# Performance work log

Hardware: AMD Instinct MI355X
Metric: run time of the kernel (lower is better)

The kernel has to match this reference:

```python
import jax, jax.numpy as jnp
import numpy as np

EPS = 1e-8        # LinearGELU eps
LN_EPS = 1e-5     # LayerNorm eps
NUM_HEADS = 16
DIM = 1024
HIDDEN = 4096
B, N = 4, 785


def _lin(x, xj, w, lw, b=None, lb=None):
    # LinearLinear: primal linear + JVP wrt input and tangent params (lw, lb)
    y = x @ w.T
    yj = xj @ w.T + x @ lw.T
    if b is not None:
        y = y + b
    if lb is not None:
        yj = yj + lb
    return y, yj


def _ln(x, xj, w, b, lw, lb):
    # LinearLayerNorm forward + manual JVP (matches torch source exactly)
    mean = x.mean(-1, keepdims=True)
    xc = x - mean
    var = (xc * xc).mean(-1, keepdims=True)
    std = jnp.sqrt(var + LN_EPS)
    xhat = xc / std
    out = xhat * w + b
    t1 = xhat * lw + lb                              # tangent wrt affine params
    mj = xj.mean(-1, keepdims=True)
    xjc = xj - mj
    a = xjc * std
    corr = 2.0 * (xc * xjc).mean(-1, keepdims=True)
    bterm = (0.5 / std) * corr * xc
    c = (1.0 / std) ** 2 * (a - bterm)
    return out, t1 + c * w


def _gelu(x, xj):
    # exact (erf) GELU; jvp uses gelu(x)/(x+EPS) + x*pdf(x) as in source
    out = 0.5 * x * (1.0 + jax.lax.erf(x * np.float32(1.0 / np.sqrt(2.0))))
    pdf = jnp.exp(-0.5 * x * x) * np.float32(1.0 / np.sqrt(2.0 * np.pi))
    return out, xj * (out / (x + EPS) + x * pdf)


def _attn(x, xj, qkv_w, qkv_lw, proj_w, proj_b, proj_lw, proj_lb):
    Bb, Nn, C = x.shape
    H = NUM_HEADS
    D = C // H
    scale = np.float32(D) ** -0.5
    qkv, qkv_j = _lin(x, xj, qkv_w, qkv_lw)  # [B,N,3C], qkv_bias=False
    def split(t):
        return t.reshape(Bb, Nn, 3, H, D).transpose(2, 0, 3, 1, 4)
    q, k, v = split(qkv)
    qj, kj, vj = split(qkv_j)
    q = q * scale
    qj = qj * scale
    attn = jax.nn.softmax(jnp.einsum('bhnd,bhmd->bhnm', q, k), axis=-1)
    out = jnp.einsum('bhnm,bhmd->bhnd', attn, v)
    # softmax JVP: dm = A_jvp + B_jvp; filter = dm*attn - rowsum(dm*attn)*attn
    dm = jnp.einsum('bhnd,bhmd->bhnm', qj, k) + jnp.einsum('bhnd,bhmd->bhnm', q, kj)
    f = dm * attn
    filt = f - f.sum(-1, keepdims=True) * attn  # == diag(dm @ attn^T) * attn correction
    out_j = jnp.einsum('bhnm,bhmd->bhnd', filt, v) + jnp.einsum('bhnm,bhmd->bhnd', attn, vj)
    out = out.transpose(0, 2, 1, 3).reshape(Bb, Nn, C)
    out_j = out_j.transpose(0, 2, 1, 3).reshape(Bb, Nn, C)
    return _lin(out, out_j, proj_w, proj_lw, proj_b, proj_lb)


def setup_inputs() -> dict:
    keys = jax.random.split(jax.random.key(0), 32)
    ki = iter(keys)
    def nrm(shape, s=0.02):
        return (jax.random.normal(next(ki), shape, jnp.float32) * s).astype(jnp.float32)
    d, h = DIM, HIDDEN
    inp = {
        'input': jax.random.normal(next(ki), (B, N, d), jnp.float32),
        'input_jvp': jax.random.normal(next(ki), (B, N, d), jnp.float32),
        'n1_w': 1.0 + nrm((d,), 0.1), 'n1_b': nrm((d,), 0.1),
        'n1_lw': nrm((d,), 0.1), 'n1_lb': nrm((d,), 0.1),
        'qkv_w': nrm((3 * d, d)), 'qkv_lw': nrm((3 * d, d)),
        'proj_w': nrm((d, d)), 'proj_b': nrm((d,), 0.1),
        'proj_lw': nrm((d, d)), 'proj_lb': nrm((d,), 0.1),
        'n2_w': 1.0 + nrm((d,), 0.1), 'n2_b': nrm((d,), 0.1),
        'n2_lw': nrm((d,), 0.1), 'n2_lb': nrm((d,), 0.1),
        'fc1_w': nrm((h, d)), 'fc1_b': nrm((h,), 0.1),
        'fc1_lw': nrm((h, d)), 'fc1_lb': nrm((h,), 0.1),
        'fc2_w': nrm((d, h)), 'fc2_b': nrm((d,), 0.1),
        'fc2_lw': nrm((d, h)), 'fc2_lb': nrm((d,), 0.1),
    }
    return inp


def reference(input, input_jvp, n1_w, n1_b, n1_lw, n1_lb, qkv_w, qkv_lw,
              proj_w, proj_b, proj_lw, proj_lb, n2_w, n2_b, n2_lw, n2_lb,
              fc1_w, fc1_b, fc1_lw, fc1_lb, fc2_w, fc2_b, fc2_lw, fc2_lb):
    x, xj = _ln(input, input_jvp, n1_w, n1_b, n1_lw, n1_lb)
    x, xj = _attn(x, xj, qkv_w, qkv_lw, proj_w, proj_b, proj_lw, proj_lb)
    x = x + input
    xj = xj + input_jvp
    i2, i2j = x, xj
    x, xj = _ln(x, xj, n2_w, n2_b, n2_lw, n2_lb)
    x, xj = _lin(x, xj, fc1_w, fc1_lw, fc1_b, fc1_lb)
    x, xj = _gelu(x, xj)
    x, xj = _lin(x, xj, fc2_w, fc2_lw, fc2_b, fc2_lb)
    return (x + i2, xj + i2j)
```

## Files before the change

kernel.cpp:

```cpp
#include <hip/hip_runtime.h>
#include <hip/hip_bf16.h>

typedef unsigned short u16;
typedef unsigned int   u32;

#define MP     3328
#define MREAL  3140
#define DIMC   1024
#define H3C    3072
#define HIDC   4096
#define NKV    785
#define SLEN   896

typedef __bf16 bf16x8 __attribute__((ext_vector_type(8)));
typedef float  f32x4  __attribute__((ext_vector_type(4)));

#define MFMA(d,a,b) (d) = __builtin_amdgcn_mfma_f32_16x16x32_bf16((a),(b),(d),0,0,0)

__device__ __forceinline__ u16 f2bf(float f){
  u32 u = __builtin_bit_cast(u32, f);
  return (u16)((u + 0x7fffu + ((u >> 16) & 1u)) >> 16);
}
__device__ __forceinline__ float bf2f(u16 h){
  return __builtin_bit_cast(float, (u32)h << 16);
}
__device__ __forceinline__ void gload16(const u16* g, u16* l){
  __builtin_amdgcn_global_load_lds(
      (const __attribute__((address_space(1))) void*)g,
      (__attribute__((address_space(3))) void*)l, 16, 0, 0);
}
__device__ __forceinline__ float wsum(float v){
  #pragma unroll
  for (int o = 32; o >= 1; o >>= 1) v += __shfl_xor(v, o);
  return v;
}

__global__ __launch_bounds__(256) void cvt_k(const float* __restrict__ in,
                                             u16* __restrict__ out, int n){
  int i = (blockIdx.x * 256 + threadIdx.x) * 4;
  if (i >= n) return;
  float4 v = *(const float4*)(in + i);
  ushort4 o4;
  o4.x = f2bf(v.x); o4.y = f2bf(v.y); o4.z = f2bf(v.z); o4.w = f2bf(v.w);
  *(ushort4*)(out + i) = o4;
}

__global__ __launch_bounds__(256) void ln_jvp_k(
    const float* __restrict__ x, const float* __restrict__ xj,
    const float* __restrict__ w, const float* __restrict__ b,
    const float* __restrict__ lw, const float* __restrict__ lb,
    u16* __restrict__ out, u16* __restrict__ outj)
{
  const int row = blockIdx.x, t = threadIdx.x;
  const size_t ro = (size_t)row * DIMC;
  if (row >= MREAL){
    for (int i = t; i < DIMC; i += 256){ out[ro+i] = 0; outj[ro+i] = 0; }
    return;
  }
  const float4 v  = ((const float4*)(x  + ro))[t];
  const float4 vj = ((const float4*)(xj + ro))[t];
  float sx  = v.x+v.y+v.z+v.w;
  float sxx = v.x*v.x+v.y*v.y+v.z*v.z+v.w*v.w;
  float sj  = vj.x+vj.y+vj.z+vj.w;
  float sxj = v.x*vj.x+v.y*vj.y+v.z*vj.z+v.w*vj.w;
  __shared__ __attribute__((aligned(64))) float red[4][4];
  sx = wsum(sx); sxx = wsum(sxx); sj = wsum(sj); sxj = wsum(sxj);
  const int wid = t>>6, lane = t&63;
  if (lane == 0){ red[wid][0]=sx; red[wid][1]=sxx; red[wid][2]=sj; red[wid][3]=sxj; }
  __syncthreads();
  sx  = red[0][0]+red[1][0]+red[2][0]+red[3][0];
  sxx = red[0][1]+red[1][1]+red[2][1]+red[3][1];
  sj  = red[0][2]+red[1][2]+red[2][2]+red[3][2];
  sxj = red[0][3]+red[1][3]+red[2][3]+red[3][3];
  const float inv  = 1.0f/1024.0f;
  const float mean = sx*inv, meanj = sj*inv;
  const float var  = sxx*inv - mean*mean;
  const float cov  = sxj*inv - mean*meanj;
  const float rstd = rsqrtf(var + 1e-5f);
  const float r3   = rstd*rstd*rstd;
  const float4 wv  = ((const float4*)w)[t];
  const float4 bv  = ((const float4*)b)[t];
  const float4 lwv = ((const float4*)lw)[t];
  const float4 lbv = ((const float4*)lb)[t];
  const float xs[4]  = {v.x,v.y,v.z,v.w},   xjs[4] = {vj.x,vj.y,vj.z,vj.w};
  const float wss[4] = {wv.x,wv.y,wv.z,wv.w}, bs[4] = {bv.x,bv.y,bv.z,bv.w};
  const float lws[4] = {lwv.x,lwv.y,lwv.z,lwv.w}, lbs[4] = {lbv.x,lbv.y,lbv.z,lbv.w};
  const int i0 = t*4;
  #pragma unroll
  for (int e = 0; e < 4; e++){
    const float xc = xs[e]-mean, xjc = xjs[e]-meanj;
    const float xhat = xc*rstd;
    const float cc = xjc*rstd - xc*cov*r3;
    out [ro+i0+e] = f2bf(xhat*wss[e] + bs[e]);
    outj[ro+i0+e] = f2bf(xhat*lws[e] + lbs[e] + cc*wss[e]);
  }
}

template<int EPI>
__global__ __launch_bounds__(512, 2) void gemm_jvp_wide_k(
    const u16* __restrict__ A, const u16* __restrict__ Aj, int lda,
    const u16* __restrict__ B, const u16* __restrict__ Bj, int K,
    const float* __restrict__ bias, const float* __restrict__ biasj,
    void* __restrict__ Yv, void* __restrict__ Yjv, int ldy)
{
  __shared__ __attribute__((aligned(128))) u16 lds[3][24576];
  const int tid = threadIdx.x, wid = tid>>6, lane = tid&63;
  const int l4 = lane>>4, l15 = lane&15;
  const int m0 = blockIdx.y*256, n0 = blockIdx.x*128;
  f32x4 accY[4][4], accJ[4][4];
  #pragma unroll
  for (int i = 0; i < 4; i++)
    #pragma unroll
    for (int j = 0; j < 4; j++){
      accY[i][j] = (f32x4){0.f,0.f,0.f,0.f};
      accJ[i][j] = (f32x4){0.f,0.f,0.f,0.f};
    }
  const int boA0 = tid*16,        boA1 = (512+tid)*16;
  const int sbA0 = boA0 ^ (((boA0>>7)&7)<<4);
  const int sbA1 = boA1 ^ (((boA1>>7)&7)<<4);
  const int rA0 = sbA0>>6, cA0 = (sbA0&63)>>1;
  const int rA1 = sbA1>>6, cA1 = (sbA1&63)>>1;
  const int boB = tid*16;
  const int sbB = boB ^ (((boB>>7)&7)<<4);
  const int rB = sbB>>6, cB = (sbB&63)>>1;
  const u16* srcA0  = A  + (size_t)(m0+rA0)*lda + cA0;
  const u16* srcA1  = A  + (size_t)(m0+rA1)*lda + cA1;
  const u16* srcAj0 = Aj + (size_t)(m0+rA0)*lda + cA0;
  const u16* srcAj1 = Aj + (size_t)(m0+rA1)*lda + cA1;
  const u16* srcB   = B  + (size_t)(n0+rB)*K + cB;
  const u16* srcBj  = Bj + (size_t)(n0+rB)*K + cB;
  const int dA0 = tid*8, dA1 = (512+tid)*8, dB = tid*8;
  const int wr = wid>>1, wc = wid&1;
  int aoff[4], boff[4];
  #pragma unroll
  for (int i = 0; i < 4; i++){
    int ab_ = (wr*64 + i*16 + l15)*64 + l4*16;
    aoff[i] = ab_ ^ (((ab_>>7)&7)<<4);
    int bb_ = (wc*64 + i*16 + l15)*64 + l4*16;
    boff[i] = bb_ ^ (((bb_>>7)&7)<<4);
  }
  auto STAGE = [&](int buf, int t){
    const int k0 = t<<5;
    u16* Lb = &lds[buf][0];
    gload16(srcA0 +k0, Lb + dA0);
    gload16(srcA1 +k0, Lb + dA1);
    gload16(srcAj0+k0, Lb + 8192 + dA0);
    gload16(srcAj1+k0, Lb + 8192 + dA1);
    gload16(srcB  +k0, Lb + 16384 + dB);
    gload16(srcBj +k0, Lb + 20480 + dB);
  };
  const int nt = K >> 5;
  STAGE(0, 0);
  STAGE(1, 1);
  for (int t = 0; t < nt; t++){
    if (t + 1 < nt) asm volatile("s_waitcnt vmcnt(6)" ::: "memory");
    else            asm volatile("s_waitcnt vmcnt(0)" ::: "memory");
    __builtin_amdgcn_s_barrier();
    if (t + 2 < nt) STAGE((t+2)%3, t+2);
    const char* Lb = (const char*)&lds[t%3][0];
    bf16x8 af[4], ajf[4], bbf[4], bjf[4];
    #pragma unroll
    for (int i = 0; i < 4; i++){
      af[i]  = *(const bf16x8*)(Lb + aoff[i]);
      ajf[i] = *(const bf16x8*)(Lb + 16384 + aoff[i]);
      bbf[i] = *(const bf16x8*)(Lb + 32768 + boff[i]);
      bjf[i] = *(const bf16x8*)(Lb + 40960 + boff[i]);
    }
    __builtin_amdgcn_s_setprio(1);
    #pragma unroll
    for (int i = 0; i < 4; i++)
      #pragma unroll
      for (int j = 0; j < 4; j++){
        MFMA(accY[i][j], af[i],  bbf[j]);
        MFMA(accJ[i][j], ajf[i], bbf[j]);
        MFMA(accJ[i][j], af[i],  bjf[j]);
      }
    __builtin_amdgcn_s_setprio(0);
  }
  const int mb = m0 + wr*64 + (l4<<2);
  const int nb = n0 + wc*64 + l15;
  #pragma unroll
  for (int i = 0; i < 4; i++)
    #pragma unroll
    for (int j = 0; j < 4; j++)
      #pragma unroll
      for (int r = 0; r < 4; r++){
        const int m = mb + i*16 + r, n = nb + j*16;
        float y = accY[i][j][r], yj = accJ[i][j][r];
        if (EPI == 0){
          ((u16*)Yv )[(size_t)m*ldy+n] = f2bf(y);
          ((u16*)Yjv)[(size_t)m*ldy+n] = f2bf(yj);
        } else {
          y  += bias[n];
          yj += biasj[n];
          const float ge  = 0.5f*y*(1.0f + erff(y*0.70710678118654752f));
          const float pdf = __expf(-0.5f*y*y)*0.3989422804014327f;
          const float gj  = yj*(ge/(y + 1e-8f) + y*pdf);
          ((u16*)Yv )[(size_t)m*ldy+n] = f2bf(ge);
          ((u16*)Yjv)[(size_t)m*ldy+n] = f2bf(gj);
        }
      }
}

template<int EPI>
__global__ __launch_bounds__(256) void gemm_jvp_k(
    const u16* __restrict__ A, const u16* __restrict__ Aj, int lda,
    const u16* __restrict__ B, const u16* __restrict__ Bj, int K,
    const float* __restrict__ bias, const float* __restrict__ biasj,
    const float* __restrict__ res, const float* __restrict__ resj,
    void* __restrict__ Yv, void* __restrict__ Yjv, int ldy, int mwrite)
{
  __shared__ __attribute__((aligned(128))) u16 lds[2][4][128*32];
  const int tid = threadIdx.x, wid = tid>>6, lane = tid&63;
  const int m0 = blockIdx.y*128, n0 = blockIdx.x*128;
  f32x4 accY[4][4], accJ[4][4];
  #pragma unroll
  for (int i = 0; i < 4; i++)
    #pragma unroll
    for (int j = 0; j < 4; j++){
      accY[i][j] = (f32x4){0.f,0.f,0.f,0.f};
      accJ[i][j] = (f32x4){0.f,0.f,0.f,0.f};
    }
  const int bo0 = wid*1024 + lane*16;
  const int bo1 = bo0 + 4096;
  const int sb0 = bo0 ^ (((bo0>>7)&7)<<4);
  const int sb1 = bo1 ^ (((bo1>>7)&7)<<4);
  const int r0 = sb0>>6, c0 = (sb0&63)>>1;
  const int r1 = sb1>>6, c1 = (sb1&63)>>1;
  const u16* A0  = A  + (size_t)(m0+r0)*lda + c0;
  const u16* A1  = A  + (size_t)(m0+r1)*lda + c1;
  const u16* Aj0 = Aj + (size_t)(m0+r0)*lda + c0;
  const u16* Aj1 = Aj + (size_t)(m0+r1)*lda + c1;
  const u16* B0  = B  + (size_t)(n0+r0)*K + c0;
  const u16* B1  = B  + (size_t)(n0+r1)*K + c1;
  const u16* Bj0 = Bj + (size_t)(n0+r0)*K + c0;
  const u16* Bj1 = Bj + (size_t)(n0+r1)*K + c1;
  const int kq = (lane>>4)<<3;
  const int ar = (wid>>1)*64 + (lane&15);
  const int bc = (wid&1)*64 + (lane&15);
  int aoff[4], boff[4];
  #pragma unroll
  for (int i = 0; i < 4; i++){
    int ab_ = (ar+i*16)*64 + (kq<<1);
    aoff[i] = ab_ ^ (((ab_>>7)&7)<<4);
    int bb_ = (bc+i*16)*64 + (kq<<1);
    boff[i] = bb_ ^ (((bb_>>7)&7)<<4);
  }
  auto STAGE = [&](int buf, int k0){
    u16* p0 = &lds[buf][0][0];
    gload16(A0 +k0, p0+(bo0>>1)); gload16(A1 +k0, p0+(bo1>>1));
    u16* p1 = &lds[buf][1][0];
    gload16(Aj0+k0, p1+(bo0>>1)); gload16(Aj1+k0, p1+(bo1>>1));
    u16* p2 = &lds[buf][2][0];
    gload16(B0 +k0, p2+(bo0>>1)); gload16(B1 +k0, p2+(bo1>>1));
    u16* p3 = &lds[buf][3][0];
    gload16(Bj0+k0, p3+(bo0>>1)); gload16(Bj1+k0, p3+(bo1>>1));
  };
  const int nt = K >> 5;
  STAGE(0, 0);
  __syncthreads();
  int cur = 0;
  for (int t = 0; t < nt; t++){
    if (t + 1 < nt) STAGE(cur^1, (t+1)<<5);
    const char* lAb  = (const char*)&lds[cur][0][0];
    const char* lAjb = (const char*)&lds[cur][1][0];
    const char* lBb  = (const char*)&lds[cur][2][0];
    const char* lBjb = (const char*)&lds[cur][3][0];
    bf16x8 af[4], ajf[4], bbf[4], bjf[4];
    #pragma unroll
    for (int i = 0; i < 4; i++){
      af[i]  = *(const bf16x8*)(lAb  + aoff[i]);
      ajf[i] = *(const bf16x8*)(lAjb + aoff[i]);
      bbf[i] = *(const bf16x8*)(lBb  + boff[i]);
      bjf[i] = *(const bf16x8*)(lBjb + boff[i]);
    }
    __builtin_amdgcn_s_setprio(1);
    #pragma unroll
    for (int i = 0; i < 4; i++)
      #pragma unroll
      for (int j = 0; j < 4; j++){
        MFMA(accY[i][j], af[i],  bbf[j]);
        MFMA(accJ[i][j], ajf[i], bbf[j]);
        MFMA(accJ[i][j], af[i],  bjf[j]);
      }
    __builtin_amdgcn_s_setprio(0);
    __syncthreads();
    cur ^= 1;
  }
  const int mb = m0 + (wid>>1)*64 + ((lane>>4)<<2);
  const int nb = n0 + (wid&1)*64 + (lane&15);
  #pragma unroll
  for (int i = 0; i < 4; i++)
    #pragma unroll
    for (int j = 0; j < 4; j++)
      #pragma unroll
      for (int r = 0; r < 4; r++){
        const int m = mb + i*16 + r, n = nb + j*16;
        float y = accY[i][j][r], yj = accJ[i][j][r];
        if (EPI == 0){
          ((u16*)Yv )[(size_t)m*ldy+n] = f2bf(y);
          ((u16*)Yjv)[(size_t)m*ldy+n] = f2bf(yj);
        } else if (EPI == 1){
          if (m < mwrite){
            y  += bias[n]  + res [(size_t)m*ldy+n];
            yj += biasj[n] + resj[(size_t)m*ldy+n];
            ((float*)Yv )[(size_t)m*ldy+n] = y;
            ((float*)Yjv)[(size_t)m*ldy+n] = yj;
          }
        } else {
          y  += bias[n];
          yj += biasj[n];
          const float ge  = 0.5f*y*(1.0f + erff(y*0.70710678118654752f));
          const float pdf = __expf(-0.5f*y*y)*0.3989422804014327f;
          const float gj  = yj*(ge/(y + 1e-8f) + y*pdf);
          ((u16*)Yv )[(size_t)m*ldy+n] = f2bf(ge);
          ((u16*)Yjv)[(size_t)m*ldy+n] = f2bf(gj);
        }
      }
}

__global__ __launch_bounds__(256) void transpose_v_k(
    const u16* __restrict__ qkvb, const u16* __restrict__ qkvjb,
    u16* __restrict__ vT, u16* __restrict__ vjT)
{
  __shared__ __attribute__((aligned(64))) u16 tl[64][80];
  __shared__ __attribute__((aligned(64))) u16 tlj[64][80];
  const int kt = blockIdx.x, bh = blockIdx.y;
  const int b = bh>>4, h = bh&15;
  const int t = threadIdx.x;
  const int kv = t>>2, dd = (t&3)*16;
  const int kvg = kt*64 + kv;
  if (kvg < NKV){
    const u16* s0 = qkvb  + (size_t)(b*NKV+kvg)*H3C + 2048 + h*64 + dd;
    const u16* s1 = qkvjb + (size_t)(b*NKV+kvg)*H3C + 2048 + h*64 + dd;
    *(uint4*)&tl [kv][dd]   = *(const uint4*)s0;
    *(uint4*)&tl [kv][dd+8] = *(const uint4*)(s0+8);
    *(uint4*)&tlj[kv][dd]   = *(const uint4*)s1;
    *(uint4*)&tlj[kv][dd+8] = *(const uint4*)(s1+8);
  } else {
    uint4 z = {0,0,0,0};
    *(uint4*)&tl [kv][dd] = z; *(uint4*)&tl [kv][dd+8] = z;
    *(uint4*)&tlj[kv][dd] = z; *(uint4*)&tlj[kv][dd+8] = z;
  }
  __syncthreads();
  const int d = t>>2, kc = (t&3)*16;
  u16* d0 = vT  + ((size_t)bh*64 + d)*SLEN + kt*64 + kc;
  u16* d1 = vjT + ((size_t)bh*64 + d)*SLEN + kt*64 + kc;
  #pragma unroll
  for (int e = 0; e < 16; e++){ d0[e] = tl[kc+e][d]; d1[e] = tlj[kc+e][d]; }
}

__global__ __launch_bounds__(256) void flash_attn_jvp_k(
    const u16* __restrict__ qkvb, const u16* __restrict__ qkvjb,
    const u16* __restrict__ vT, const u16* __restrict__ vjT,
    u16* __restrict__ o, u16* __restrict__ oj)
{
  __shared__ __attribute__((aligned(64))) u16 lK  [64*64];
  __shared__ __attribute__((aligned(64))) u16 lKj [64*64];
  __shared__ __attribute__((aligned(64))) u16 lvT [64*64];
  __shared__ __attribute__((aligned(64))) u16 lvjT[64*64];
  __shared__ __attribute__((aligned(64))) u16 pl  [128*64];
  __shared__ __attribute__((aligned(64))) u16 pdl [128*64];
  const int tid = threadIdx.x, wid = tid>>6, lane = tid&63;
  const int l4 = lane>>4, l15 = lane&15;
  const int qt = blockIdx.x, bh = blockIdx.y, b = bh>>4, h = bh&15;

  bf16x8 qf[2][2], qjf[2][2];
  {
    const size_t qrb = (size_t)b*NKV + qt*128 + wid*32;
    #pragma unroll
    for (int i = 0; i < 2; i++){
      const size_t ro = (qrb + i*16 + l15)*H3C + h*64;
      #pragma unroll
      for (int ks = 0; ks < 2; ks++){
        qf [i][ks] = *(const bf16x8*)(qkvb  + ro + ks*32 + l4*8);
        qjf[i][ks] = *(const bf16x8*)(qkvjb + ro + ks*32 + l4*8);
      }
    }
  }
  float m_st[2][4], l_st[2][4], g_st[2][4];
  f32x4 PO[2][4], PTJ[2][4];
  #pragma unroll
  for (int i = 0; i < 2; i++)
    #pragma unroll
    for (int r = 0; r < 4; r++){
      m_st[i][r] = -1e30f; l_st[i][r] = 0.f; g_st[i][r] = 0.f;
    }
  #pragma unroll
  for (int i = 0; i < 2; i++)
    #pragma unroll
    for (int j = 0; j < 4; j++){
      PO[i][j] = (f32x4){0.f,0.f,0.f,0.f};
      PTJ[i][j] = (f32x4){0.f,0.f,0.f,0.f};
    }
  const char* lKb   = (const char*)lK;
  const char* lKjb  = (const char*)lKj;
  const char* lvTb  = (const char*)lvT;
  const char* lvjTb = (const char*)lvjT;
  char* plb  = (char*)pl;
  char* pdlb = (char*)pdl;

  for (int t = 0; t < 13; t++){
    #pragma unroll
    for (int rnd = 0; rnd < 2; rnd++){
      const int gidx = rnd*256 + tid;
      const int row = gidx>>3, c = gidx&7;
      const int cs = c ^ (row&7);
      const size_t ksrc = (size_t)(b*NKV + t*64 + row)*H3C + 1024 + h*64 + cs*8;
      gload16(qkvb  + ksrc, lK  + gidx*8);
      gload16(qkvjb + ksrc, lKj + gidx*8);
      const size_t vsrc = ((size_t)bh*64 + row)*SLEN + t*64 + cs*8;
      gload16(vT  + vsrc, lvT  + gidx*8);
      gload16(vjT + vsrc, lvjT + gidx*8);
    }
    __syncthreads();

    #pragma unroll
    for (int i = 0; i < 2; i++){
      f32x4 s[4], dm[4];
      #pragma unroll
      for (int j = 0; j < 4; j++){
        s[j] = (f32x4){0.f,0.f,0.f,0.f};
        dm[j] = (f32x4){0.f,0.f,0.f,0.f};
      }
      #pragma unroll
      for (int ks = 0; ks < 2; ks++){
        #pragma unroll
        for (int j = 0; j < 4; j++){
          const int row = j*16 + l15;
          const int byt = (row*128 + ks*64 + l4*16) ^ ((row&7)<<4);
          const bf16x8 kf  = *(const bf16x8*)(lKb  + byt);
          const bf16x8 kjf = *(const bf16x8*)(lKjb + byt);
          MFMA(s[j],  qf[i][ks],  kf);
          MFMA(dm[j], qjf[i][ks], kf);
          MFMA(dm[j], qf[i][ks],  kjf);
        }
      }
      float tm[4] = {-1e30f,-1e30f,-1e30f,-1e30f};
      #pragma unroll
      for (int j = 0; j < 4; j++){
        const int colg = t*64 + j*16 + l15;
        #pragma unroll
        for (int r = 0; r < 4; r++){
          float sv = s[j][r]*0.125f;
          if (colg >= NKV) sv = -1e30f;
          s[j][r] = sv;
          dm[j][r] *= 0.125f;
          tm[r] = fmaxf(tm[r], sv);
        }
      }
      #pragma unroll
      for (int r = 0; r < 4; r++){
        float v = tm[r];
        v = fmaxf(v, __shfl_xor(v, 1));
        v = fmaxf(v, __shfl_xor(v, 2));
        v = fmaxf(v, __shfl_xor(v, 4));
        v = fmaxf(v, __shfl_xor(v, 8));
        const float mn = fmaxf(m_st[i][r], v);
        const float sc = __expf(m_st[i][r] - mn);
        m_st[i][r] = mn;
        l_st[i][r] *= sc;
        g_st[i][r] *= sc;
        #pragma unroll
        for (int j = 0; j < 4; j++){ PO[i][j][r] *= sc; PTJ[i][j][r] *= sc; }
      }
      float ps[4] = {0.f,0.f,0.f,0.f}, pds[4] = {0.f,0.f,0.f,0.f};
      #pragma unroll
      for (int j = 0; j < 4; j++){
        const int col = j*16 + l15;
        #pragma unroll
        for (int r = 0; r < 4; r++){
          const float p  = __expf(s[j][r] - m_st[i][r]);
          const float pd = p * dm[j][r];
          ps[r] += p; pds[r] += pd;
          const int row = wid*32 + i*16 + l4*4 + r;
          const int byt = (row*128 + col*2) ^ ((row&7)<<4);
          *(u16*)(plb  + byt) = f2bf(p);
          *(u16*)(pdlb + byt) = f2bf(pd);
        }
      }
      #pragma unroll
      for (int r = 0; r < 4; r++){
        float v = ps[r], w = pds[r];
        v += __shfl_xor(v, 1); w += __shfl_xor(w, 1);
        v += __shfl_xor(v, 2); w += __shfl_xor(w, 2);
        v += __shfl_xor(v, 4); w += __shfl_xor(w, 4);
        v += __shfl_xor(v, 8); w += __shfl_xor(w, 8);
        l_st[i][r] += v; g_st[i][r] += w;
      }
    }

    #pragma unroll
    for (int ks = 0; ks < 2; ks++){
      bf16x8 pa[2], pda[2];
      #pragma unroll
      for (int i = 0; i < 2; i++){
        const int row = wid*32 + i*16 + l15;
        const int byt = (row*128 + ks*64 + l4*16) ^ ((row&7)<<4);
        pa[i]  = *(const bf16x8*)(plb  + byt);
        pda[i] = *(const bf16x8*)(pdlb + byt);
      }
      #pragma unroll
      for (int j = 0; j < 4; j++){
        const int row = j*16 + l15;
        const int byt = (row*128 + ks*64 + l4*16) ^ ((row&7)<<4);
        const bf16x8 vb  = *(const bf16x8*)(lvTb  + byt);
        const bf16x8 vjb = *(const bf16x8*)(lvjTb + byt);
        #pragma unroll
        for (int i = 0; i < 2; i++){
          MFMA(PO[i][j],  pa[i],  vb);
          MFMA(PTJ[i][j], pda[i], vb);
          MFMA(PTJ[i][j], pa[i],  vjb);
        }
      }
    }
    __syncthreads();
  }

  #pragma unroll
  for (int i = 0; i < 2; i++)
    #pragma unroll
    for (int r = 0; r < 4; r++){
      const int ql = qt*128 + wid*32 + i*16 + l4*4 + r;
      if (ql < NKV){
        const float rl = 1.0f / l_st[i][r];
        const float gg = g_st[i][r] * rl;
        #pragma unroll
        for (int j = 0; j < 4; j++){
          const size_t oo = ((size_t)b*NKV + ql)*DIMC + h*64 + j*16 + l15;
          const float po = PO[i][j][r] * rl;
          o [oo] = f2bf(po);
          oj[oo] = f2bf(PTJ[i][j][r]*rl - gg*po);
        }
      }
    }
}

extern "C" void kernel_launch(void* const* d_in, const int* in_sizes, int n_in,
                              void* d_out, int out_size, void* d_ws, size_t ws_size,
                              hipStream_t stream)
{
  (void)in_sizes; (void)n_in; (void)out_size;
  const float* input   = (const float*)d_in[0];
  const float* inputj  = (const float*)d_in[1];
  const float* n1_w    = (const float*)d_in[2];
  const float* n1_b    = (const float*)d_in[3];
  const float* n1_lw   = (const float*)d_in[4];
  const float* n1_lb   = (const float*)d_in[5];
  const float* qkv_w   = (const float*)d_in[6];
  const float* qkv_lw  = (const float*)d_in[7];
  const float* proj_w  = (const float*)d_in[8];
  const float* proj_b  = (const float*)d_in[9];
  const float* proj_lw = (const float*)d_in[10];
  const float* proj_lb = (const float*)d_in[11];
  const float* n2_w    = (const float*)d_in[12];
  const float* n2_b    = (const float*)d_in[13];
  const float* n2_lw   = (const float*)d_in[14];
  const float* n2_lb   = (const float*)d_in[15];
  const float* fc1_w   = (const float*)d_in[16];
  const float* fc1_b   = (const float*)d_in[17];
  const float* fc1_lw  = (const float*)d_in[18];
  const float* fc1_lb  = (const float*)d_in[19];
  const float* fc2_w   = (const float*)d_in[20];
  const float* fc2_b   = (const float*)d_in[21];
  const float* fc2_lw  = (const float*)d_in[22];
  const float* fc2_lb  = (const float*)d_in[23];

  const size_t SZ_W      = 2u*4194304u*2u;
  const size_t SZ_ARENA1 = 2u*(size_t)MP*HIDC*2u;
  const size_t SZ_VT     = (size_t)64*64*SLEN*2u;
  const size_t SZ_ARENA2 = 2u*SZ_VT;
  const size_t SZ_ARENA3 = 2u*(size_t)MP*DIMC*2u;
  const size_t SZ_X2     = (size_t)MP*DIMC*4u;
  const size_t NEEDED = SZ_W + SZ_ARENA1 + SZ_ARENA2 + SZ_ARENA3 + 2u*SZ_X2 + 4096u;
  if (ws_size < NEEDED) return;

  char* base = (char*)d_ws;
  size_t off = 0;
  auto ab = [&](size_t bytes)->char*{
    char* p = base + off;
    off += bytes; off = (off + 255) & ~(size_t)255;
    return p;
  };
  char* Wslot  = ab(SZ_W);
  char* arena1 = ab(SZ_ARENA1);
  char* arena2 = ab(SZ_ARENA2);
  char* arena3 = ab(SZ_ARENA3);
  float* x2  = (float*)ab(SZ_X2);
  float* x2j = (float*)ab(SZ_X2);

  u16* wbuf  = (u16*)Wslot;
  u16* wjbuf = wbuf + 4194304;
  u16* qkvb  = (u16*)arena1;
  u16* qkvjb = qkvb + (size_t)MP*H3C;
  u16* hb    = (u16*)arena1;
  u16* hjb   = hb + (size_t)MP*HIDC;
  u16* vT    = (u16*)arena2;
  u16* vjT   = vT + (size_t)64*64*SLEN;
  u16* x3b   = (u16*)arena2;
  u16* x3jb  = x3b + (size_t)MP*DIMC;
  u16* x1b   = (u16*)arena3;
  u16* x1jb  = x1b + (size_t)MP*DIMC;
  u16* ob    = (u16*)arena3;
  u16* ojb   = ob + (size_t)MP*DIMC;

  auto cvt = [&](const float* src, u16* dst, int n){
    cvt_k<<<dim3((n + 1023)/1024), 256, 0, stream>>>(src, dst, n);
  };

  ln_jvp_k<<<dim3(MP), 256, 0, stream>>>(input, inputj, n1_w, n1_b, n1_lw, n1_lb,
                                         x1b, x1jb);
  cvt(qkv_w, wbuf, H3C*DIMC); cvt(qkv_lw, wjbuf, H3C*DIMC);
  gemm_jvp_wide_k<0><<<dim3(H3C/128, MP/256), 512, 0, stream>>>(
      x1b, x1jb, DIMC, wbuf, wjbuf, DIMC, nullptr, nullptr,
      qkvb, qkvjb, H3C);
  transpose_v_k<<<dim3(14, 64), 256, 0, stream>>>(qkvb, qkvjb, vT, vjT);
  flash_attn_jvp_k<<<dim3(7, 64), 256, 0, stream>>>(qkvb, qkvjb, vT, vjT, ob, ojb);
  cvt(proj_w, wbuf, DIMC*DIMC); cvt(proj_lw, wjbuf, DIMC*DIMC);
  gemm_jvp_k<1><<<dim3(DIMC/128, MP/128), 256, 0, stream>>>(
      ob, ojb, DIMC, wbuf, wjbuf, DIMC, proj_b, proj_lb, input, inputj,
      x2, x2j, DIMC, MREAL);
  ln_jvp_k<<<dim3(MP), 256, 0, stream>>>(x2, x2j, n2_w, n2_b, n2_lw, n2_lb,
                                         x3b, x3jb);
  cvt(fc1_w, wbuf, HIDC*DIMC); cvt(fc1_lw, wjbuf, HIDC*DIMC);
  gemm_jvp_wide_k<2><<<dim3(HIDC/128, MP/256), 512, 0, stream>>>(
      x3b, x3jb, DIMC, wbuf, wjbuf, DIMC, fc1_b, fc1_lb,
      hb, hjb, HIDC);
  cvt(fc2_w, wbuf, DIMC*HIDC); cvt(fc2_lw, wjbuf, DIMC*HIDC);
  float* out0 = (float*)d_out;
  float* out1 = out0 + (size_t)MREAL*DIMC;
  gemm_jvp_k<1><<<dim3(DIMC/128, MP/128), 256, 0, stream>>>(
      hb, hjb, HIDC, wbuf, wjbuf, HIDC, fc2_b, fc2_lb, x2, x2j,
      out0, out1, DIMC, MREAL);
}
```

Before: 572.4 us.

## Interleave global loads with three MFMA phases in wide JVP GEMM main loop

Splits each K-step of the JVP GEMM into three MFMA phases (Y, J from Aj, J from Bj). Each phase's LDS fragment reads and next-stage global loads are interleaved between the phases, with barriers in between, so memory traffic overlaps MFMA work. It also drops the launch-bounds occupancy hint from 2 to 1 block per CU, giving the compiler more registers. The cost is many more barriers per iteration and possibly lower occupancy. The reordered wait and barrier logic also risks subtle race or stall issues.

```diff
diff --git a/kernel.cpp b/kernel.cpp
--- a/kernel.cpp
+++ b/kernel.cpp
@@ -97,7 +97,7 @@
 }
 
 template<int EPI>
-__global__ __launch_bounds__(512, 2) void gemm_jvp_wide_k(
+__global__ __launch_bounds__(512, 1) void gemm_jvp_wide_k(
     const u16* __restrict__ A, const u16* __restrict__ Aj, int lda,
     const u16* __restrict__ B, const u16* __restrict__ Bj, int K,
     const float* __restrict__ bias, const float* __restrict__ biasj,
@@ -139,7 +139,7 @@
     int bb_ = (wc*64 + i*16 + l15)*64 + l4*16;
     boff[i] = bb_ ^ (((bb_>>7)&7)<<4);
   }
-  auto STAGE = [&](int buf, int t){
+  auto STAGE_ALL = [&](int buf, int t){
     const int k0 = t<<5;
     u16* Lb = &lds[buf][0];
     gload16(srcA0 +k0, Lb + dA0);
@@ -150,32 +150,60 @@
     gload16(srcBj +k0, Lb + 20480 + dB);
   };
   const int nt = K >> 5;
-  STAGE(0, 0);
-  STAGE(1, 1);
+  STAGE_ALL(0, 0);
+  STAGE_ALL(1, 1);
+  asm volatile("s_waitcnt vmcnt(6)" ::: "memory");
+  __builtin_amdgcn_s_barrier();
   for (int t = 0; t < nt; t++){
-    if (t + 1 < nt) asm volatile("s_waitcnt vmcnt(6)" ::: "memory");
-    else            asm volatile("s_waitcnt vmcnt(0)" ::: "memory");
-    __builtin_amdgcn_s_barrier();
-    if (t + 2 < nt) STAGE((t+2)%3, t+2);
     const char* Lb = (const char*)&lds[t%3][0];
+    const int sbuf = (t+2)%3;
+    const int sk0  = (t+2)<<5;
+    u16* Sb = &lds[sbuf][0];
+    const bool st = (t + 2 < nt);
     bf16x8 af[4], ajf[4], bbf[4], bjf[4];
     #pragma unroll
     for (int i = 0; i < 4; i++){
       af[i]  = *(const bf16x8*)(Lb + aoff[i]);
+      bbf[i] = *(const bf16x8*)(Lb + 32768 + boff[i]);
+    }
+    if (st){ gload16(srcA0+sk0, Sb + dA0); gload16(srcA1+sk0, Sb + dA1); }
+    __builtin_amdgcn_s_barrier();
+    __builtin_amdgcn_s_setprio(1);
+    #pragma unroll
+    for (int i = 0; i < 4; i++)
+      #pragma unroll
+      for (int j = 0; j < 4; j++)
+        MFMA(accY[i][j], af[i], bbf[j]);
+    __builtin_amdgcn_s_setprio(0);
+    __builtin_amdgcn_s_barrier();
+    #pragma unroll
+    for (int i = 0; i < 4; i++)
       ajf[i] = *(const bf16x8*)(Lb + 16384 + aoff[i]);
-      bbf[i] = *(const bf16x8*)(Lb + 32768 + boff[i]);
-      bjf[i] = *(const bf16x8*)(Lb + 40960 + boff[i]);
-    }
+    if (st){ gload16(srcAj0+sk0, Sb + 8192 + dA0); gload16(srcAj1+sk0, Sb + 8192 + dA1); }
+    __builtin_amdgcn_s_barrier();
     __builtin_amdgcn_s_setprio(1);
     #pragma unroll
     for (int i = 0; i < 4; i++)
       #pragma unroll
-      for (int j = 0; j < 4; j++){
-        MFMA(accY[i][j], af[i],  bbf[j]);
+      for (int j = 0; j < 4; j++)
         MFMA(accJ[i][j], ajf[i], bbf[j]);
-        MFMA(accJ[i][j], af[i],  bjf[j]);
-      }
     __builtin_amdgcn_s_setprio(0);
+    __builtin_amdgcn_s_barrier();
+    #pragma unroll
+    for (int j = 0; j < 4; j++)
+      bjf[j] = *(const bf16x8*)(Lb + 40960 + boff[j]);
+    if (st){ gload16(srcB+sk0, Sb + 16384 + dB); gload16(srcBj+sk0, Sb + 20480 + dB); }
+    if (st)                  asm volatile("s_waitcnt vmcnt(6)" ::: "memory");
+    else if (t + 1 < nt)     asm volatile("s_waitcnt vmcnt(0)" ::: "memory");
+    __builtin_amdgcn_s_barrier();
+    __builtin_amdgcn_s_setprio(1);
+    #pragma unroll
+    for (int i = 0; i < 4; i++)
+      #pragma unroll
+      for (int j = 0; j < 4; j++)
+        MFMA(accJ[i][j], af[i], bjf[j]);
+    __builtin_amdgcn_s_setprio(0);
+    __builtin_amdgcn_s_barrier();
   }
   const int mb = m0 + wr*64 + (l4<<2);
   const int nb = n0 + wc*64 + l15;
```

Measured after the change: 578.3 us. No clear change (+1.0%).
